# Performance work log

Measured on AMD Instinct MI355X. Metric: run time of the kernel, lower is better.

The kernel has to match this reference:

```python
import jax, jax.numpy as jnp
import numpy as np
from jax import lax

B, T, F, H = 128, 4096, 64, 128

def setup_inputs() -> dict:
    key = jax.random.key(0)
    k1, k2, k3, k4, k5 = jax.random.split(key, 5)
    s = 1.0 / np.sqrt(H)  # PyTorch LSTM init scale
    X = jax.random.normal(k1, (B, T, F), dtype=jnp.float32)
    W_ih = jax.random.uniform(k2, (4 * H, F), minval=-s, maxval=s, dtype=jnp.float32)
    W_hh = jax.random.uniform(k3, (4 * H, H), minval=-s, maxval=s, dtype=jnp.float32)
    b_ih = jax.random.uniform(k4, (4 * H,), minval=-s, maxval=s, dtype=jnp.float32)
    b_hh = jax.random.uniform(k5, (4 * H,), minval=-s, maxval=s, dtype=jnp.float32)
    return {"X": X, "W_ih": W_ih, "W_hh": W_hh, "b_ih": b_ih, "b_hh": b_hh}

def reference(X, W_ih, W_hh, b_ih, b_hh):
    # Faithful to the torch module: per-sequence LSTM with zero init state,
    # returning the output at the final timestep (== final hidden state).
    # PyTorch gate order: i, f, g, o.
    Bn, Tn, _ = X.shape
    Hn = W_hh.shape[1]
    # Precompute input contribution for all timesteps: [B, T, 4H]
    xg = jnp.einsum('btf,gf->btg', X, W_ih) + b_ih + b_hh
    xg_t = jnp.swapaxes(xg, 0, 1)  # [T, B, 4H]

    def step(carry, xg_step):
        h, c = carry
        gates = xg_step + h @ W_hh.T  # [B, 4H]
        i, f, g, o = jnp.split(gates, 4, axis=-1)
        i = jax.nn.sigmoid(i)
        f = jax.nn.sigmoid(f)
        g = jnp.tanh(g)
        o = jax.nn.sigmoid(o)
        c = f * c + i * g
        h = o * jnp.tanh(c)
        return (h, c), None

    h0 = jnp.zeros((Bn, Hn), dtype=X.dtype)
    c0 = jnp.zeros((Bn, Hn), dtype=X.dtype)
    (h_last, _), _ = lax.scan(step, (h0, c0), xg_t)
    return h_last  # [B, H]: the torch code's list of (1,1,H) outs, stacked
```

## Files before the change

kernel.cpp:

```cpp
#include <hip/hip_runtime.h>

#define B_  128
#define T_  4096
#define F_  64
#define H_  128
#define NT  512

typedef _Float16 half8_t __attribute__((ext_vector_type(8)));
typedef _Float16 half2_t __attribute__((ext_vector_type(2)));
typedef float    f32x4   __attribute__((ext_vector_type(4)));

__device__ __forceinline__ half2_t pack2(float a, float b) {
  half2_t r; r[0] = (_Float16)a; r[1] = (_Float16)b; return r;
}

__device__ __forceinline__ void wg_barrier() {
  __asm__ volatile("s_waitcnt lgkmcnt(0)\n\ts_barrier" ::: "memory");
}

__device__ __forceinline__ float fast_sigmoid(float x) {
  float e = __builtin_amdgcn_exp2f(x * -1.4426950408889634f);
  return __builtin_amdgcn_rcpf(1.0f + e);
}
__device__ __forceinline__ float fast_tanh(float x) {
  float e = __builtin_amdgcn_exp2f(x * -2.8853900817779268f);
  return 2.0f * __builtin_amdgcn_rcpf(1.0f + e) - 1.0f;
}

__global__ __launch_bounds__(NT, 2) void lstm_xg_kernel(
    const float* __restrict__ X,
    const float* __restrict__ Wih,
    const float* __restrict__ Whh,
    const float* __restrict__ bih,
    const float* __restrict__ bhh,
    float* __restrict__ out)
{
  const int tid  = threadIdx.x;
  const int b    = blockIdx.x;
  const int lane = tid & 63;
  const int w    = tid >> 6;
  const int lg   = lane >> 4;
  const int lc   = lane & 15;

  __shared__ __align__(16) _Float16 hbuf[2][H_];
  __shared__ __align__(16) _Float16 xst[2][16 * 72];
  __shared__ __align__(16) float    xg[2][16 * 512];

  half8_t Wf[4][6];
  f32x4   xinit[4];
#pragma unroll
  for (int g = 0; g < 4; ++g) {
    const int row = 128 * g + 16 * w + lc;
    const float bv = bih[row] + bhh[row];
    f32x4 bi = {bv, bv, bv, bv};
    xinit[g] = bi;
#pragma unroll
    for (int c = 0; c < 6; ++c) {
      const float* src = (c < 4) ? (Whh + (size_t)row * H_ + 32 * c + 8 * lg)
                                 : (Wih + (size_t)row * F_ + 32 * (c - 4) + 8 * lg);
      float4 lo = *(const float4*)(src);
      float4 hi = *(const float4*)(src + 4);
      half8_t v;
      v[0] = (_Float16)lo.x; v[1] = (_Float16)lo.y;
      v[2] = (_Float16)lo.z; v[3] = (_Float16)lo.w;
      v[4] = (_Float16)hi.x; v[5] = (_Float16)hi.y;
      v[6] = (_Float16)hi.z; v[7] = (_Float16)hi.w;
      Wf[g][c] = v;
    }
  }

  const float* xbase = X + (size_t)b * T_ * F_;
  const int    tp    = tid >> 5;
  const int    kp    = tid & 31;

  {
    float2 v0 = ((const float2*)xbase)[0 * 512 + tid];
    float2 v1 = ((const float2*)xbase)[1 * 512 + tid];
    *(half2_t*)&xst[0][tp * 72 + 2 * kp] = pack2(v0.x, v0.y);
    *(half2_t*)&xst[1][tp * 72 + 2 * kp] = pack2(v1.x, v1.y);
  }
  wg_barrier();

  const f32x4 zf = {0.0f, 0.0f, 0.0f, 0.0f};

  {
    half8_t a0 = *(const half8_t*)&xst[0][lc * 72 + 8 * lg];
    half8_t a1 = *(const half8_t*)&xst[0][lc * 72 + 32 + 8 * lg];
#pragma unroll
    for (int g = 0; g < 4; ++g) {
      f32x4 ab = __builtin_amdgcn_mfma_f32_16x16x32_f16(a0, Wf[g][4], xinit[g], 0, 0, 0);
      ab       = __builtin_amdgcn_mfma_f32_16x16x32_f16(a1, Wf[g][5], ab, 0, 0, 0);
      if (g == 0) { xinit[0] = xinit[0]; }
#pragma unroll
      for (int r = 0; r < 4; ++r)
        xg[0][(4 * lg + r) * 512 + (16 * w + lc) * 4 + g] = ab[r];
    }
  }
  wg_barrier();

  f32x4 pre[4], pB[4];
#pragma unroll
  for (int g = 0; g < 4; ++g) { pre[g] = zf; pB[g] = zf; }
  f32x4 xg4 = *(const f32x4*)&xg[0][0 * 512 + (16 * w + lc) * 4];

  float cs = 0.0f, hl = 0.0f;
  float2 xv = {0.0f, 0.0f};

#pragma unroll 2
  for (int t = 0; t < T_; ++t) {
    const int buf = t & 1;
    const int P   = t >> 4;
    const int tau = t & 15;

    float si = fast_sigmoid(pre[0][0] + pB[0][0] + xg4[0]);
    float sf = fast_sigmoid(pre[1][0] + pB[1][0] + xg4[1]);
    float sg = fast_tanh   (pre[2][0] + pB[2][0] + xg4[2]);
    float so = fast_sigmoid(pre[3][0] + pB[3][0] + xg4[3]);

    cs = sf * cs + si * sg;
    float hn = so * fast_tanh(cs);
    hl = hn;

    if (lane < 16) hbuf[buf][16 * w + lc] = (_Float16)hn;

    if (tau == 0) {
      const int sb = (P + 1) & 1;
      half8_t a0 = *(const half8_t*)&xst[sb][lc * 72 + 8 * lg];
      half8_t a1 = *(const half8_t*)&xst[sb][lc * 72 + 32 + 8 * lg];
#pragma unroll
      for (int g = 0; g < 4; ++g) {
        f32x4 ab = __builtin_amdgcn_mfma_f32_16x16x32_f16(a0, Wf[g][4], xinit[g], 0, 0, 0);
        ab       = __builtin_amdgcn_mfma_f32_16x16x32_f16(a1, Wf[g][5], ab, 0, 0, 0);
#pragma unroll
        for (int r = 0; r < 4; ++r)
          xg[sb][(4 * lg + r) * 512 + (16 * w + lc) * 4 + g] = ab[r];
      }
      int Pn = P + 2; if (Pn > (T_ / 16 - 1)) Pn = T_ / 16 - 1;
      xv = ((const float2*)xbase)[(size_t)Pn * 512 + tid];
    }
    if (tau == 8) {
      *(half2_t*)&xst[P & 1][tp * 72 + 2 * kp] = pack2(xv.x, xv.y);
    }

    wg_barrier();

    half8_t ah0 = *(const half8_t*)&hbuf[buf][ 0 + 8 * lg];
    half8_t ah1 = *(const half8_t*)&hbuf[buf][32 + 8 * lg];
    half8_t ah2 = *(const half8_t*)&hbuf[buf][64 + 8 * lg];
    half8_t ah3 = *(const half8_t*)&hbuf[buf][96 + 8 * lg];

    const int tn = t + 1;
    xg4 = *(const f32x4*)&xg[(tn >> 4) & 1][(tn & 15) * 512 + (16 * w + lc) * 4];

#pragma unroll
    for (int g = 0; g < 4; ++g) {
      f32x4 a  = __builtin_amdgcn_mfma_f32_16x16x32_f16(ah0, Wf[g][0], zf, 0, 0, 0);
      pre[g]   = __builtin_amdgcn_mfma_f32_16x16x32_f16(ah1, Wf[g][1], a, 0, 0, 0);
      f32x4 a2 = __builtin_amdgcn_mfma_f32_16x16x32_f16(ah2, Wf[g][2], zf, 0, 0, 0);
      pB[g]    = __builtin_amdgcn_mfma_f32_16x16x32_f16(ah3, Wf[g][3], a2, 0, 0, 0);
    }
  }

  if (lane < 16) out[(size_t)b * H_ + 16 * w + lc] = hl;
}

extern "C" void kernel_launch(void* const* d_in, const int* in_sizes, int n_in,
                              void* d_out, int out_size, void* d_ws, size_t ws_size,
                              hipStream_t stream) {
  const float* X   = (const float*)d_in[0];
  const float* Wih = (const float*)d_in[1];
  const float* Whh = (const float*)d_in[2];
  const float* bih = (const float*)d_in[3];
  const float* bhh = (const float*)d_in[4];
  float* out = (float*)d_out;

  lstm_xg_kernel<<<dim3(B_), dim3(NT), 0, stream>>>(X, Wih, Whh, bih, bhh, out);
}
```

Before: 1.947 ms.

## Spread input-projection MFMAs across timesteps, pad xg LDS, reorder recurrent MFMAs

The per-chunk input projection, which ran all four gates at tau==0, is now spread over tau 0..3 at one gate per step. Its A operands are preloaded into registers at tau==15, and the global X load moves to tau==4. The xg row stride is padded to 516 to reduce LDS bank conflicts. The xg4 load for the next step moves before the barrier. The recurrent MFMAs are reordered so independent chains interleave, which hides MFMA dependency latency on the serial critical path. Together these aim to even out per-step latency spikes, at the cost of holding extra registers live.

```diff
diff --git a/kernel.cpp b/kernel.cpp
--- a/kernel.cpp
+++ b/kernel.cpp
@@ -5,6 +5,7 @@
 #define F_  64
 #define H_  128
 #define NT  512
+#define XGS 516
 
 typedef _Float16 half8_t __attribute__((ext_vector_type(8)));
 typedef _Float16 half2_t __attribute__((ext_vector_type(2)));
@@ -27,7 +28,7 @@
   return 2.0f * __builtin_amdgcn_rcpf(1.0f + e) - 1.0f;
 }
 
-__global__ __launch_bounds__(NT, 2) void lstm_xg_kernel(
+__global__ __launch_bounds__(NT, 2) void lstm_xg2_kernel(
     const float* __restrict__ X,
     const float* __restrict__ Wih,
     const float* __restrict__ Whh,
@@ -44,7 +45,7 @@
 
   __shared__ __align__(16) _Float16 hbuf[2][H_];
   __shared__ __align__(16) _Float16 xst[2][16 * 72];
-  __shared__ __align__(16) float    xg[2][16 * 512];
+  __shared__ __align__(16) float    xg[2][16 * XGS];
 
   half8_t Wf[4][6];
   f32x4   xinit[4];
@@ -90,18 +91,19 @@
     for (int g = 0; g < 4; ++g) {
       f32x4 ab = __builtin_amdgcn_mfma_f32_16x16x32_f16(a0, Wf[g][4], xinit[g], 0, 0, 0);
       ab       = __builtin_amdgcn_mfma_f32_16x16x32_f16(a1, Wf[g][5], ab, 0, 0, 0);
-      if (g == 0) { xinit[0] = xinit[0]; }
 #pragma unroll
       for (int r = 0; r < 4; ++r)
-        xg[0][(4 * lg + r) * 512 + (16 * w + lc) * 4 + g] = ab[r];
+        xg[0][(4 * lg + r) * XGS + (16 * w + lc) * 4 + g] = ab[r];
     }
   }
+  half8_t ga0 = *(const half8_t*)&xst[1][lc * 72 + 8 * lg];
+  half8_t ga1 = *(const half8_t*)&xst[1][lc * 72 + 32 + 8 * lg];
   wg_barrier();
 
   f32x4 pre[4], pB[4];
 #pragma unroll
   for (int g = 0; g < 4; ++g) { pre[g] = zf; pB[g] = zf; }
-  f32x4 xg4 = *(const f32x4*)&xg[0][0 * 512 + (16 * w + lc) * 4];
+  f32x4 xg4 = *(const f32x4*)&xg[0][0 * XGS + (16 * w + lc) * 4];
 
   float cs = 0.0f, hl = 0.0f;
   float2 xv = {0.0f, 0.0f};
@@ -123,23 +125,28 @@
 
     if (lane < 16) hbuf[buf][16 * w + lc] = (_Float16)hn;
 
-    if (tau == 0) {
+    if (tau < 4) {
       const int sb = (P + 1) & 1;
-      half8_t a0 = *(const half8_t*)&xst[sb][lc * 72 + 8 * lg];
-      half8_t a1 = *(const half8_t*)&xst[sb][lc * 72 + 32 + 8 * lg];
+      const int g  = tau;
+      f32x4 ab = __builtin_amdgcn_mfma_f32_16x16x32_f16(ga0, Wf[g][4], xinit[g], 0, 0, 0);
+      ab       = __builtin_amdgcn_mfma_f32_16x16x32_f16(ga1, Wf[g][5], ab, 0, 0, 0);
 #pragma unroll
-      for (int g = 0; g < 4; ++g) {
-        f32x4 ab = __builtin_amdgcn_mfma_f32_16x16x32_f16(a0, Wf[g][4], xinit[g], 0, 0, 0);
-        ab       = __builtin_amdgcn_mfma_f32_16x16x32_f16(a1, Wf[g][5], ab, 0, 0, 0);
-#pragma unroll
-        for (int r = 0; r < 4; ++r)
-          xg[sb][(4 * lg + r) * 512 + (16 * w + lc) * 4 + g] = ab[r];
-      }
+      for (int r = 0; r < 4; ++r)
+        xg[sb][(4 * lg + r) * XGS + (16 * w + lc) * 4 + g] = ab[r];
+    } else if (tau == 4) {
       int Pn = P + 2; if (Pn > (T_ / 16 - 1)) Pn = T_ / 16 - 1;
       xv = ((const float2*)xbase)[(size_t)Pn * 512 + tid];
+    } else if (tau == 8) {
+      *(half2_t*)&xst[P & 1][tp * 72 + 2 * kp] = pack2(xv.x, xv.y);
+    } else if (tau == 15) {
+      const int sn = P & 1;
+      ga0 = *(const half8_t*)&xst[sn][lc * 72 + 8 * lg];
+      ga1 = *(const half8_t*)&xst[sn][lc * 72 + 32 + 8 * lg];
     }
-    if (tau == 8) {
-      *(half2_t*)&xst[P & 1][tp * 72 + 2 * kp] = pack2(xv.x, xv.y);
+
+    {
+      const int tn = t + 1;
+      xg4 = *(const f32x4*)&xg[(tn >> 4) & 1][(tn & 15) * XGS + (16 * w + lc) * 4];
     }
 
     wg_barrier();
@@ -149,16 +156,19 @@
     half8_t ah2 = *(const half8_t*)&hbuf[buf][64 + 8 * lg];
     half8_t ah3 = *(const half8_t*)&hbuf[buf][96 + 8 * lg];
 
-    const int tn = t + 1;
-    xg4 = *(const f32x4*)&xg[(tn >> 4) & 1][(tn & 15) * 512 + (16 * w + lc) * 4];
-
+    f32x4 aA[4], aB[4];
 #pragma unroll
-    for (int g = 0; g < 4; ++g) {
-      f32x4 a  = __builtin_amdgcn_mfma_f32_16x16x32_f16(ah0, Wf[g][0], zf, 0, 0, 0);
-      pre[g]   = __builtin_amdgcn_mfma_f32_16x16x32_f16(ah1, Wf[g][1], a, 0, 0, 0);
-      f32x4 a2 = __builtin_amdgcn_mfma_f32_16x16x32_f16(ah2, Wf[g][2], zf, 0, 0, 0);
-      pB[g]    = __builtin_amdgcn_mfma_f32_16x16x32_f16(ah3, Wf[g][3], a2, 0, 0, 0);
-    }
+    for (int g = 0; g < 4; ++g)
+      aA[g] = __builtin_amdgcn_mfma_f32_16x16x32_f16(ah0, Wf[g][0], zf, 0, 0, 0);
+#pragma unroll
+    for (int g = 0; g < 4; ++g)
+      aB[g] = __builtin_amdgcn_mfma_f32_16x16x32_f16(ah2, Wf[g][2], zf, 0, 0, 0);
+#pragma unroll
+    for (int g = 0; g < 4; ++g)
+      pre[g] = __builtin_amdgcn_mfma_f32_16x16x32_f16(ah1, Wf[g][1], aA[g], 0, 0, 0);
+#pragma unroll
+    for (int g = 0; g < 4; ++g)
+      pB[g]  = __builtin_amdgcn_mfma_f32_16x16x32_f16(ah3, Wf[g][3], aB[g], 0, 0, 0);
   }
 
   if (lane < 16) out[(size_t)b * H_ + 16 * w + lc] = hl;
@@ -174,5 +184,5 @@
   const float* bhh = (const float*)d_in[4];
   float* out = (float*)d_out;
 
-  lstm_xg_kernel<<<dim3(B_), dim3(NT), 0, stream>>>(X, Wih, Whh, bih, bhh, out);
+  lstm_xg2_kernel<<<dim3(B_), dim3(NT), 0, stream>>>(X, Wih, Whh, bih, bhh, out);
 }
```

After: 2.762 ms. 1.42x slower.
